# Optimization experiments

Hardware: AMD Instinct MI355X
Metric: run time of the kernel (lower is better)

## Reference

```python
import jax, jax.numpy as jnp
import numpy as np

EPS = 1e-5
SLOPE = 0.01  # torch LeakyReLU default negative_slope


def _stage(h, W):
    # h: [B, N, k, Cin]; W: [Cout, Cin] (1x1 conv, no bias)
    h = jnp.einsum('bnkc,oc->bnko', h, W)
    # InstanceNorm2d (affine=False): normalize per (batch, channel) over spatial (N, k)
    mean = jnp.mean(h, axis=(1, 2), keepdims=True)
    var = jnp.var(h, axis=(1, 2), keepdims=True)
    h = (h - mean) * jax.lax.rsqrt(var + EPS)
    return jnp.where(h >= 0, h, SLOPE * h)


def setup_inputs() -> dict:
    key = jax.random.key(0)
    k1, k2, k3, k4, k5 = jax.random.split(key, 5)
    B, N, D, K, C = 8, 4096, 64, 20, 64
    x = jax.random.normal(k1, (B, N, D), dtype=jnp.float32)
    ind = jax.random.randint(k2, (B, N, K), 0, B * N, dtype=jnp.int64)
    W1 = jax.random.normal(k3, (C, 2 * D), dtype=jnp.float32) * 0.05
    W2 = jax.random.normal(k4, (C, C), dtype=jnp.float32) * 0.05
    W3 = jax.random.normal(k5, (C, C), dtype=jnp.float32) * 0.05
    return {"x": x, "ind": ind, "W1": W1, "W2": W2, "W3": W3}


def reference(x, ind, W1, W2, W3):
    B, N, D = x.shape
    k = ind.shape[2]
    # Gather neighbors via global (B*N) indices, as in the torch code
    y = x.reshape(B * N, D)[ind.reshape(B * N, k)].reshape(B, N, k, D)  # [B,N,k,D]
    xe = jnp.broadcast_to(x[:, :, None, :], (B, N, k, D))
    feat = jnp.concatenate([y - xe, xe], axis=3)  # [B,N,k,2D]
    h = _stage(feat, W1)
    h = _stage(h, W2)
    h = _stage(h, W3)
    # max-pool over k neighbors -> [B, N, Cout]
    return jnp.max(h, axis=2)
```

## Files before the change

kernel.cpp:

```cpp
#include <hip/hip_runtime.h>

#define BDIM 8
#define NPTS 4096
#define KNEI 20
#define BN (BDIM*NPTS)
#define NKCNT (NPTS*KNEI)
#define EPSI 1e-5f
#define SLOPE 0.01f

typedef _Float16 half_t;
typedef __attribute__((ext_vector_type(2))) _Float16 h2v;
typedef __attribute__((ext_vector_type(4))) _Float16 h4v;
typedef __attribute__((ext_vector_type(8))) _Float16 h8v;
typedef __attribute__((ext_vector_type(4))) float f32x4;
typedef __attribute__((ext_vector_type(2))) float f32x2;

__device__ __forceinline__ h2v cvt2(float a, float b) {
    return __builtin_bit_cast(h2v, __builtin_amdgcn_cvt_pkrtz(a, b));
}
__device__ __forceinline__ unsigned long long pack4_f16(const f32x4& a) {
    unsigned p0 = __builtin_bit_cast(unsigned, cvt2(a[0], a[1]));
    unsigned p1 = __builtin_bit_cast(unsigned, cvt2(a[2], a[3]));
    return ((unsigned long long)p1 << 32) | p0;
}

__global__ __launch_bounds__(256) void k0_uv(const float* __restrict__ x,
        const float* __restrict__ W1, const float* __restrict__ W2,
        const float* __restrict__ W3, half_t* __restrict__ u,
        half_t* __restrict__ v, half_t* __restrict__ Wh2,
        half_t* __restrict__ Wh3) {
    int tid = threadIdx.x;
    if (blockIdx.x >= BN / 64) {
        const float* src = (blockIdx.x == BN / 64) ? W2 : W3;
        half_t* dst = (blockIdx.x == BN / 64) ? Wh2 : Wh3;
        for (int i = tid; i < 4096; i += 256) dst[i] = (half_t)src[i];
        return;
    }
    int lane = tid & 63, w = tid >> 6;
    int l15 = lane & 15, q = lane >> 4;
    int row = blockIdx.x * 64 + w * 16 + l15;
    h8v bx[2];
#pragma unroll
    for (int kc = 0; kc < 2; ++kc) {
        const float* xp = x + (size_t)row * 64 + kc * 32 + q * 8;
        f32x4 x0 = *(const f32x4*)xp;
        f32x4 x1 = *(const f32x4*)(xp + 4);
        h8v t;
#pragma unroll
        for (int j = 0; j < 4; ++j) { t[j] = (half_t)x0[j]; t[4 + j] = (half_t)x1[j]; }
        bx[kc] = t;
    }
    h8v wa[4][2], wd[4][2];
#pragma unroll
    for (int mt = 0; mt < 4; ++mt)
#pragma unroll
        for (int kc = 0; kc < 2; ++kc) {
            const float* wp = W1 + (mt * 16 + l15) * 128 + kc * 32 + q * 8;
            f32x4 a0 = *(const f32x4*)wp;
            f32x4 a1 = *(const f32x4*)(wp + 4);
            f32x4 b0 = *(const f32x4*)(wp + 64);
            f32x4 b1 = *(const f32x4*)(wp + 68);
            h8v ta, td;
#pragma unroll
            for (int j = 0; j < 4; ++j) {
                ta[j] = (half_t)a0[j]; ta[4 + j] = (half_t)a1[j];
                td[j] = (half_t)(b0[j] - a0[j]); td[4 + j] = (half_t)(b1[j] - a1[j]);
            }
            wa[mt][kc] = ta; wd[mt][kc] = td;
        }
#pragma unroll
    for (int mt = 0; mt < 4; ++mt) {
        f32x4 au = {0.f, 0.f, 0.f, 0.f}, av = {0.f, 0.f, 0.f, 0.f};
        au = __builtin_amdgcn_mfma_f32_16x16x32_f16(wa[mt][0], bx[0], au, 0, 0, 0);
        au = __builtin_amdgcn_mfma_f32_16x16x32_f16(wa[mt][1], bx[1], au, 0, 0, 0);
        av = __builtin_amdgcn_mfma_f32_16x16x32_f16(wd[mt][0], bx[0], av, 0, 0, 0);
        av = __builtin_amdgcn_mfma_f32_16x16x32_f16(wd[mt][1], bx[1], av, 0, 0, 0);
        *(unsigned long long*)(u + (size_t)row * 64 + mt * 16 + q * 4) = pack4_f16(au);
        *(unsigned long long*)(v + (size_t)row * 64 + mt * 16 + q * 4) = pack4_f16(av);
    }
}

__global__ __launch_bounds__(256) void k1_stats1(const half_t* __restrict__ u,
        const half_t* __restrict__ v, const int* __restrict__ ind,
        float* __restrict__ s1) {
    __shared__ float sacc[128];
    int tid = threadIdx.x;
    if (tid < 128) sacc[tid] = 0.f;
    int lane = tid & 63, w = tid >> 6;
    int b = blockIdx.x >> 8;
    int n0 = (blockIdx.x & 255) << 4;
    int p = b * NPTS + n0 + w * 4 + (lane >> 4);
    int rh = (lane >> 3) & 1, c8 = lane & 7;
    const int* ip = ind + (size_t)p * 20;
    int idx[10];
#pragma unroll
    for (int r = 0; r < 10; ++r) idx[r] = ip[r * 2 + rh];
    h8v vv = *(const h8v*)(v + (size_t)p * 64 + c8 * 8);
    h8v g[10];
#pragma unroll
    for (int r = 0; r < 10; ++r)
        g[r] = *(const h8v*)(u + (size_t)idx[r] * 64 + c8 * 8);
    float s[8] = {}, qa[8] = {};
#pragma unroll
    for (int r = 0; r < 10; ++r) {
        h8v h = g[r] + vv;
#pragma unroll
        for (int j = 0; j < 8; ++j) {
            float f = (float)h[j];
            s[j] += f; qa[j] = fmaf(f, f, qa[j]);
        }
    }
#pragma unroll
    for (int m = 8; m <= 32; m <<= 1)
#pragma unroll
        for (int j = 0; j < 8; ++j) {
            s[j] += __shfl_xor(s[j], m, 64);
            qa[j] += __shfl_xor(qa[j], m, 64);
        }
    __syncthreads();
    if ((lane & 56) == 0) {
#pragma unroll
        for (int j = 0; j < 8; ++j) {
            atomicAdd(&sacc[c8 * 8 + j], s[j]);
            atomicAdd(&sacc[64 + c8 * 8 + j], qa[j]);
        }
    }
    __syncthreads();
    if (tid < 128)
        atomicAdd(&s1[(tid >> 6) * 512 + b * 64 + (tid & 63)], sacc[tid]);
}

__global__ __launch_bounds__(256, 3) void k2_stats2(const half_t* __restrict__ u,
        const half_t* __restrict__ v, const int* __restrict__ ind,
        const half_t* __restrict__ Wh2, const float* __restrict__ s1,
        float* __restrict__ s2) {
    __shared__ float sacc[128];
    int tid = threadIdx.x;
    if (tid < 128) sacc[tid] = 0.f;
    int lane = tid & 63, w = tid >> 6;
    int l15 = lane & 15, q = lane >> 4;
    int b = blockIdx.x >> 8;
    int n0 = (blockIdx.x & 255) << 4;
    int base = b * NPTS + n0;
    int base20 = base * 20;
    int idxs[5];
#pragma unroll
    for (int nt = 0; nt < 5; ++nt)
        idxs[nt] = ind[base20 + w * 80 + l15 * 5 + nt];
    const half_t* up0 = u + (size_t)idxs[0] * 64 + q * 8;
    h8v cu0 = *(const h8v*)up0;
    h8v cu1 = *(const h8v*)(up0 + 32);
    int gp = base + w * 4 + (l15 >> 2);
    h8v vfr[2];
#pragma unroll
    for (int kc = 0; kc < 2; ++kc)
        vfr[kc] = *(const h8v*)(v + (size_t)gp * 64 + kc * 32 + q * 8);
    h8v aw[4][2];
#pragma unroll
    for (int mt = 0; mt < 4; ++mt)
#pragma unroll
        for (int kc = 0; kc < 2; ++kc)
            aw[mt][kc] = *(const h8v*)(Wh2 + (mt * 16 + l15) * 64 + kc * 32 + q * 8);
    const float inv = 1.0f / (float)NKCNT;
    h8v r1v[2], vn[2];
#pragma unroll
    for (int kc = 0; kc < 2; ++kc)
#pragma unroll
        for (int j = 0; j < 8; ++j) {
            int c = kc * 32 + q * 8 + j;
            float mm = s1[b * 64 + c] * inv;
            float va = s1[512 + b * 64 + c] * inv - mm * mm;
            float rs = rsqrtf(va + EPSI);
            r1v[kc][j] = (half_t)rs;
            vn[kc][j] = (half_t)(((float)vfr[kc][j] - mm) * rs);
        }
    float ss[4][4] = {}, sq[4][4] = {};
#pragma unroll
    for (int nt = 0; nt < 5; ++nt) {
        h8v nx0, nx1;
        if (nt < 4) {
            const half_t* upn = u + (size_t)idxs[nt + 1] * 64 + q * 8;
            nx0 = *(const h8v*)upn;
            nx1 = *(const h8v*)(upn + 32);
        }
        h8v t0 = cu0 * r1v[0] + vn[0];
        h8v t1 = cu1 * r1v[1] + vn[1];
        h8v b0 = __builtin_elementwise_max(t0, t0 * (half_t)SLOPE);
        h8v b1 = __builtin_elementwise_max(t1, t1 * (half_t)SLOPE);
#pragma unroll
        for (int mt = 0; mt < 4; ++mt) {
            f32x4 a = {0.f, 0.f, 0.f, 0.f};
            a = __builtin_amdgcn_mfma_f32_16x16x32_f16(aw[mt][0], b0, a, 0, 0, 0);
            a = __builtin_amdgcn_mfma_f32_16x16x32_f16(aw[mt][1], b1, a, 0, 0, 0);
#pragma unroll
            for (int j = 0; j < 4; ++j) {
                ss[mt][j] += a[j];
                sq[mt][j] = fmaf(a[j], a[j], sq[mt][j]);
            }
        }
        if (nt < 4) { cu0 = nx0; cu1 = nx1; }
    }
#pragma unroll
    for (int m = 1; m < 16; m <<= 1)
#pragma unroll
        for (int mt = 0; mt < 4; ++mt)
#pragma unroll
            for (int j = 0; j < 4; ++j) {
                ss[mt][j] += __shfl_xor(ss[mt][j], m, 64);
                sq[mt][j] += __shfl_xor(sq[mt][j], m, 64);
            }
    __syncthreads();
    if (l15 == 0) {
#pragma unroll
        for (int mt = 0; mt < 4; ++mt)
#pragma unroll
            for (int j = 0; j < 4; ++j) {
                atomicAdd(&sacc[mt * 16 + q * 4 + j], ss[mt][j]);
                atomicAdd(&sacc[64 + mt * 16 + q * 4 + j], sq[mt][j]);
            }
    }
    __syncthreads();
    if (tid < 128)
        atomicAdd(&s2[(tid >> 6) * 512 + b * 64 + (tid & 63)], sacc[tid]);
}

__global__ __launch_bounds__(256, 3) void k3_fused(const half_t* __restrict__ u,
        const half_t* __restrict__ v, const int* __restrict__ ind,
        const half_t* __restrict__ Wh2, const half_t* __restrict__ Wh3,
        const float* __restrict__ s1, const float* __restrict__ s2,
        float* __restrict__ s3, float* __restrict__ out) {
    __shared__ __align__(16) unsigned char wlds[16384];
    __shared__ __align__(16) unsigned char scr[16384];
    __shared__ float sacc[128];
    int tid = threadIdx.x;
    if (tid < 128) sacc[tid] = 0.f;
    int lane = tid & 63, w = tid >> 6;
    int l15 = lane & 15, q = lane >> 4;
    int rw7 = l15 & 7;
    int b = blockIdx.x >> 8;
    int n0 = (blockIdx.x & 255) << 4;
    int base = b * NPTS + n0;
    int base20 = base * 20;
    for (int i = tid; i < 512; i += 256) {
        int rw = i >> 3, ch = i & 7;
        *(h8v*)(wlds + rw * 128 + ((ch ^ (rw & 7)) << 4)) =
            *(const h8v*)(Wh2 + rw * 64 + ch * 8);
        *(h8v*)(wlds + 8192 + rw * 128 + ((ch ^ (rw & 7)) << 4)) =
            *(const h8v*)(Wh3 + rw * 64 + ch * 8);
    }
    int idxs[5];
#pragma unroll
    for (int nt = 0; nt < 5; ++nt)
        idxs[nt] = ind[base20 + w * 80 + l15 * 5 + nt];
    const half_t* up0 = u + (size_t)idxs[0] * 64 + q * 8;
    h8v cu0 = *(const h8v*)up0;
    h8v cu1 = *(const h8v*)(up0 + 32);
    int gp = base + w * 4 + (l15 >> 2);
    h8v vfr[2];
#pragma unroll
    for (int kc = 0; kc < 2; ++kc)
        vfr[kc] = *(const h8v*)(v + (size_t)gp * 64 + kc * 32 + q * 8);
    const float inv = 1.0f / (float)NKCNT;
    h8v r1v[2], vn[2], r2v[2], m2v[2];
#pragma unroll
    for (int kc = 0; kc < 2; ++kc)
#pragma unroll
        for (int j = 0; j < 8; ++j) {
            int c = kc * 32 + q * 8 + j;
            float mm = s1[b * 64 + c] * inv;
            float va = s1[512 + b * 64 + c] * inv - mm * mm;
            float rs = rsqrtf(va + EPSI);
            r1v[kc][j] = (half_t)rs;
            vn[kc][j] = (half_t)(((float)vfr[kc][j] - mm) * rs);
            float mm2 = s2[b * 64 + c] * inv;
            float va2 = s2[512 + b * 64 + c] * inv - mm2 * mm2;
            float rs2 = rsqrtf(va2 + EPSI);
            r2v[kc][j] = (half_t)rs2;
            m2v[kc][j] = (half_t)(-mm2 * rs2);
        }
    unsigned char* scrw0 = scr + w * 4096;
    __syncthreads();
    float ss[4][4] = {}, sq[4][4] = {};
    h2v pm[4][2];
#pragma unroll
    for (int mt = 0; mt < 4; ++mt)
#pragma unroll
        for (int r = 0; r < 2; ++r)
            pm[mt][r] = (h2v){(half_t)-65504.f, (half_t)-65504.f};
#pragma unroll
    for (int nt = 0; nt < 6; ++nt) {
        if (nt < 5) {
            h8v nx0, nx1;
            if (nt < 4) {
                const half_t* upn = u + (size_t)idxs[nt + 1] * 64 + q * 8;
                nx0 = *(const h8v*)upn;
                nx1 = *(const h8v*)(upn + 32);
            }
            unsigned char* scrw = scrw0 + (nt & 1) * 2048;
            h8v t0 = cu0 * r1v[0] + vn[0];
            h8v t1 = cu1 * r1v[1] + vn[1];
            h8v b0 = __builtin_elementwise_max(t0, t0 * (half_t)SLOPE);
            h8v b1 = __builtin_elementwise_max(t1, t1 * (half_t)SLOPE);
#pragma unroll
            for (int mt = 0; mt < 4; ++mt) {
                h8v w0 = *(const h8v*)(wlds + (mt * 16 + l15) * 128 + ((q ^ rw7) << 4));
                h8v w1 = *(const h8v*)(wlds + (mt * 16 + l15) * 128 + (((4 + q) ^ rw7) << 4));
                f32x4 a = {0.f, 0.f, 0.f, 0.f};
                a = __builtin_amdgcn_mfma_f32_16x16x32_f16(w0, b0, a, 0, 0, 0);
                a = __builtin_amdgcn_mfma_f32_16x16x32_f16(w1, b1, a, 0, 0, 0);
                *(unsigned long long*)(scrw + l15 * 128 +
                    (((mt * 2 + (q >> 1)) ^ rw7) << 4) + (q & 1) * 8) = pack4_f16(a);
            }
            if (nt < 4) { cu0 = nx0; cu1 = nx1; }
        }
        if (nt > 0) {
            int m = nt - 1;
            unsigned char* scrr = scrw0 + (m & 1) * 2048;
            h8v hr0 = *(const h8v*)(scrr + l15 * 128 + ((q ^ rw7) << 4));
            h8v hr1 = *(const h8v*)(scrr + l15 * 128 + (((4 + q) ^ rw7) << 4));
            h8v t0 = hr0 * r2v[0] + m2v[0];
            h8v t1 = hr1 * r2v[1] + m2v[1];
            h8v b0 = __builtin_elementwise_max(t0, t0 * (half_t)SLOPE);
            h8v b1 = __builtin_elementwise_max(t1, t1 * (half_t)SLOPE);
#pragma unroll
            for (int mt = 0; mt < 4; ++mt) {
                h8v w0 = *(const h8v*)(wlds + 8192 + (mt * 16 + l15) * 128 + ((q ^ rw7) << 4));
                h8v w1 = *(const h8v*)(wlds + 8192 + (mt * 16 + l15) * 128 + (((4 + q) ^ rw7) << 4));
                f32x4 a = {0.f, 0.f, 0.f, 0.f};
                a = __builtin_amdgcn_mfma_f32_16x16x32_f16(w0, b0, a, 0, 0, 0);
                a = __builtin_amdgcn_mfma_f32_16x16x32_f16(w1, b1, a, 0, 0, 0);
#pragma unroll
                for (int j = 0; j < 4; ++j) {
                    ss[mt][j] += a[j];
                    sq[mt][j] = fmaf(a[j], a[j], sq[mt][j]);
                }
                h2v p0 = cvt2(a[0], a[1]);
                h2v p1 = cvt2(a[2], a[3]);
                pm[mt][0] = __builtin_elementwise_max(pm[mt][0], p0);
                pm[mt][1] = __builtin_elementwise_max(pm[mt][1], p1);
            }
        }
    }
#pragma unroll
    for (int m = 1; m <= 2; m <<= 1)
#pragma unroll
        for (int mt = 0; mt < 4; ++mt)
#pragma unroll
            for (int r = 0; r < 2; ++r) {
                int t = __shfl_xor(__builtin_bit_cast(int, pm[mt][r]), m, 64);
                pm[mt][r] = __builtin_elementwise_max(pm[mt][r],
                               __builtin_bit_cast(h2v, t));
            }
    {
        int ms = l15 & 3;
        h2v sa = ms == 0 ? pm[0][0] : ms == 1 ? pm[1][0] : ms == 2 ? pm[2][0] : pm[3][0];
        h2v sb = ms == 0 ? pm[0][1] : ms == 1 ? pm[1][1] : ms == 2 ? pm[2][1] : pm[3][1];
        f32x4 o = {(float)sa[0], (float)sa[1], (float)sb[0], (float)sb[1]};
        *(f32x4*)(out + (size_t)gp * 64 + ms * 16 + q * 4) = o;
    }
#pragma unroll
    for (int m = 1; m < 16; m <<= 1)
#pragma unroll
        for (int mt = 0; mt < 4; ++mt)
#pragma unroll
            for (int j = 0; j < 4; ++j) {
                ss[mt][j] += __shfl_xor(ss[mt][j], m, 64);
                sq[mt][j] += __shfl_xor(sq[mt][j], m, 64);
            }
    if (l15 == 0) {
#pragma unroll
        for (int mt = 0; mt < 4; ++mt)
#pragma unroll
            for (int j = 0; j < 4; ++j) {
                atomicAdd(&sacc[mt * 16 + q * 4 + j], ss[mt][j]);
                atomicAdd(&sacc[64 + mt * 16 + q * 4 + j], sq[mt][j]);
            }
    }
    __syncthreads();
    if (tid < 128)
        atomicAdd(&s3[(tid >> 6) * 512 + b * 64 + (tid & 63)], sacc[tid]);
}

__global__ __launch_bounds__(256) void k4_final(float* __restrict__ out,
        const float* __restrict__ s3) {
    int idx = blockIdx.x * 256 + threadIdx.x;
    int c = idx & 63;
    int b = idx >> 18;
    const float inv = 1.0f / (float)NKCNT;
    float mm = s3[b * 64 + c] * inv;
    float vv = s3[512 + b * 64 + c] * inv - mm * mm;
    float r = rsqrtf(vv + EPSI);
    float val = (out[idx] - mm) * r;
    out[idx] = val >= 0.f ? val : SLOPE * val;
}

extern "C" void kernel_launch(void* const* d_in, const int* in_sizes, int n_in,
                              void* d_out, int out_size, void* d_ws, size_t ws_size,
                              hipStream_t stream) {
    const float* x   = (const float*)d_in[0];
    const int*   ind = (const int*)d_in[1];
    const float* W1  = (const float*)d_in[2];
    const float* W2  = (const float*)d_in[3];
    const float* W3  = (const float*)d_in[4];
    float* out = (float*)d_out;

    half_t* u   = (half_t*)d_ws;
    half_t* v   = u + (size_t)BN * 64;
    half_t* Wh2 = v + (size_t)BN * 64;
    half_t* Wh3 = Wh2 + 4096;
    float* stats = (float*)(Wh3 + 4096);
    float* s1 = stats;
    float* s2 = stats + 1024;
    float* s3 = stats + 2048;

    (void)hipMemsetAsync(stats, 0, 3 * 1024 * sizeof(float), stream);
    k0_uv<<<dim3(BN / 64 + 2), dim3(256), 0, stream>>>(x, W1, W2, W3, u, v, Wh2, Wh3);
    k1_stats1<<<dim3(BN / 16), dim3(256), 0, stream>>>(u, v, ind, s1);
    k2_stats2<<<dim3(BN / 16), dim3(256), 0, stream>>>(u, v, ind, Wh2, s1, s2);
    k3_fused<<<dim3(BN / 16), dim3(256), 0, stream>>>(u, v, ind, Wh2, Wh3, s1, s2, s3, out);
    k4_final<<<dim3(BN * 64 / 256), dim3(256), 0, stream>>>(out, s3);
}
```

Measured before the change: 180.0 us.

## Process two point groups per block with cross-group prefetch in gather kernels

Each block of the three gather kernels now handles two consecutive 16-point groups, so half as many blocks are launched. This amortises the weight loads, the LDS weight staging and the per-block stat atomics. The next group's indices, v rows and first u rows are prefetched during the current group's loop to hide gather latency. The cost is more live registers, which may lower occupancy, and fewer blocks to fill the GPU.

```diff
diff --git a/kernel.cpp b/kernel.cpp
--- a/kernel.cpp
+++ b/kernel.cpp
@@ -87,27 +87,41 @@
     int tid = threadIdx.x;
     if (tid < 128) sacc[tid] = 0.f;
     int lane = tid & 63, w = tid >> 6;
-    int b = blockIdx.x >> 8;
-    int n0 = (blockIdx.x & 255) << 4;
-    int p = b * NPTS + n0 + w * 4 + (lane >> 4);
+    int g0 = blockIdx.x * 2;
+    int b = g0 >> 8;
     int rh = (lane >> 3) & 1, c8 = lane & 7;
-    const int* ip = ind + (size_t)p * 20;
+    int p0 = b * NPTS + ((g0 & 255) << 4) + w * 4 + (lane >> 4);
+    const int* ip = ind + (size_t)p0 * 20;
     int idx[10];
 #pragma unroll
     for (int r = 0; r < 10; ++r) idx[r] = ip[r * 2 + rh];
-    h8v vv = *(const h8v*)(v + (size_t)p * 64 + c8 * 8);
-    h8v g[10];
-#pragma unroll
-    for (int r = 0; r < 10; ++r)
-        g[r] = *(const h8v*)(u + (size_t)idx[r] * 64 + c8 * 8);
     float s[8] = {}, qa[8] = {};
-#pragma unroll
-    for (int r = 0; r < 10; ++r) {
-        h8v h = g[r] + vv;
-#pragma unroll
-        for (int j = 0; j < 8; ++j) {
-            float f = (float)h[j];
-            s[j] += f; qa[j] = fmaf(f, f, qa[j]);
+#pragma unroll 1
+    for (int g = 0; g < 2; ++g) {
+        int p = p0 + g * 16;
+        h8v vv = *(const h8v*)(v + (size_t)p * 64 + c8 * 8);
+        h8v gg[10];
+#pragma unroll
+        for (int r = 0; r < 10; ++r)
+            gg[r] = *(const h8v*)(u + (size_t)idx[r] * 64 + c8 * 8);
+        int idxn[10];
+        if (g == 0) {
+            const int* ipn = ind + (size_t)(p0 + 16) * 20;
+#pragma unroll
+            for (int r = 0; r < 10; ++r) idxn[r] = ipn[r * 2 + rh];
+        }
+#pragma unroll
+        for (int r = 0; r < 10; ++r) {
+            h8v h = gg[r] + vv;
+#pragma unroll
+            for (int j = 0; j < 8; ++j) {
+                float f = (float)h[j];
+                s[j] += f; qa[j] = fmaf(f, f, qa[j]);
+            }
+        }
+        if (g == 0) {
+#pragma unroll
+            for (int r = 0; r < 10; ++r) idx[r] = idxn[r];
         }
     }
 #pragma unroll
@@ -139,22 +153,9 @@
     if (tid < 128) sacc[tid] = 0.f;
     int lane = tid & 63, w = tid >> 6;
     int l15 = lane & 15, q = lane >> 4;
-    int b = blockIdx.x >> 8;
-    int n0 = (blockIdx.x & 255) << 4;
-    int base = b * NPTS + n0;
-    int base20 = base * 20;
-    int idxs[5];
-#pragma unroll
-    for (int nt = 0; nt < 5; ++nt)
-        idxs[nt] = ind[base20 + w * 80 + l15 * 5 + nt];
-    const half_t* up0 = u + (size_t)idxs[0] * 64 + q * 8;
-    h8v cu0 = *(const h8v*)up0;
-    h8v cu1 = *(const h8v*)(up0 + 32);
-    int gp = base + w * 4 + (l15 >> 2);
-    h8v vfr[2];
-#pragma unroll
-    for (int kc = 0; kc < 2; ++kc)
-        vfr[kc] = *(const h8v*)(v + (size_t)gp * 64 + kc * 32 + q * 8);
+    int g0 = blockIdx.x * 2;
+    int b = g0 >> 8;
+    int base0 = b * NPTS + ((g0 & 255) << 4);
     h8v aw[4][2];
 #pragma unroll
     for (int mt = 0; mt < 4; ++mt)
@@ -162,43 +163,77 @@
         for (int kc = 0; kc < 2; ++kc)
             aw[mt][kc] = *(const h8v*)(Wh2 + (mt * 16 + l15) * 64 + kc * 32 + q * 8);
     const float inv = 1.0f / (float)NKCNT;
-    h8v r1v[2], vn[2];
-#pragma unroll
-    for (int kc = 0; kc < 2; ++kc)
-#pragma unroll
-        for (int j = 0; j < 8; ++j) {
-            int c = kc * 32 + q * 8 + j;
-            float mm = s1[b * 64 + c] * inv;
-            float va = s1[512 + b * 64 + c] * inv - mm * mm;
-            float rs = rsqrtf(va + EPSI);
-            r1v[kc][j] = (half_t)rs;
-            vn[kc][j] = (half_t)(((float)vfr[kc][j] - mm) * rs);
-        }
+    int idxs[5];
+#pragma unroll
+    for (int nt = 0; nt < 5; ++nt)
+        idxs[nt] = ind[(size_t)base0 * 20 + w * 80 + l15 * 5 + nt];
+    const half_t* upi = u + (size_t)idxs[0] * 64 + q * 8;
+    h8v cu0 = *(const h8v*)upi;
+    h8v cu1 = *(const h8v*)(upi + 32);
+    int gp0 = base0 + w * 4 + (l15 >> 2);
+    h8v vfr[2];
+    vfr[0] = *(const h8v*)(v + (size_t)gp0 * 64 + q * 8);
+    vfr[1] = *(const h8v*)(v + (size_t)gp0 * 64 + 32 + q * 8);
     float ss[4][4] = {}, sq[4][4] = {};
-#pragma unroll
-    for (int nt = 0; nt < 5; ++nt) {
-        h8v nx0, nx1;
-        if (nt < 4) {
-            const half_t* upn = u + (size_t)idxs[nt + 1] * 64 + q * 8;
-            nx0 = *(const h8v*)upn;
-            nx1 = *(const h8v*)(upn + 32);
-        }
-        h8v t0 = cu0 * r1v[0] + vn[0];
-        h8v t1 = cu1 * r1v[1] + vn[1];
-        h8v b0 = __builtin_elementwise_max(t0, t0 * (half_t)SLOPE);
-        h8v b1 = __builtin_elementwise_max(t1, t1 * (half_t)SLOPE);
-#pragma unroll
-        for (int mt = 0; mt < 4; ++mt) {
-            f32x4 a = {0.f, 0.f, 0.f, 0.f};
-            a = __builtin_amdgcn_mfma_f32_16x16x32_f16(aw[mt][0], b0, a, 0, 0, 0);
-            a = __builtin_amdgcn_mfma_f32_16x16x32_f16(aw[mt][1], b1, a, 0, 0, 0);
-#pragma unroll
-            for (int j = 0; j < 4; ++j) {
-                ss[mt][j] += a[j];
-                sq[mt][j] = fmaf(a[j], a[j], sq[mt][j]);
-            }
-        }
-        if (nt < 4) { cu0 = nx0; cu1 = nx1; }
+#pragma unroll 1
+    for (int g = 0; g < 2; ++g) {
+        h8v r1v[2], vn[2];
+#pragma unroll
+        for (int kc = 0; kc < 2; ++kc)
+#pragma unroll
+            for (int j = 0; j < 8; ++j) {
+                int c = kc * 32 + q * 8 + j;
+                float mm = s1[b * 64 + c] * inv;
+                float va = s1[512 + b * 64 + c] * inv - mm * mm;
+                float rs = rsqrtf(va + EPSI);
+                r1v[kc][j] = (half_t)rs;
+                vn[kc][j] = (half_t)(((float)vfr[kc][j] - mm) * rs);
+            }
+        int idxs_n[5];
+        h8v cun0, cun1, vfn0, vfn1;
+#pragma unroll
+        for (int nt = 0; nt < 5; ++nt) {
+            h8v nx0, nx1;
+            if (nt < 4) {
+                const half_t* upn = u + (size_t)idxs[nt + 1] * 64 + q * 8;
+                nx0 = *(const h8v*)upn;
+                nx1 = *(const h8v*)(upn + 32);
+            }
+            if (nt == 0 && g == 0) {
+#pragma unroll
+                for (int r = 0; r < 5; ++r)
+                    idxs_n[r] = ind[(size_t)(base0 + 16) * 20 + w * 80 + l15 * 5 + r];
+                vfn0 = *(const h8v*)(v + (size_t)(gp0 + 16) * 64 + q * 8);
+                vfn1 = *(const h8v*)(v + (size_t)(gp0 + 16) * 64 + 32 + q * 8);
+            }
+            if (nt == 4 && g == 0) {
+                const half_t* upn = u + (size_t)idxs_n[0] * 64 + q * 8;
+                cun0 = *(const h8v*)upn;
+                cun1 = *(const h8v*)(upn + 32);
+            }
+            h8v t0 = cu0 * r1v[0] + vn[0];
+            h8v t1 = cu1 * r1v[1] + vn[1];
+            h8v b0 = __builtin_elementwise_max(t0, t0 * (half_t)SLOPE);
+            h8v b1 = __builtin_elementwise_max(t1, t1 * (half_t)SLOPE);
+#pragma unroll
+            for (int mt = 0; mt < 4; ++mt) {
+                f32x4 a = {0.f, 0.f, 0.f, 0.f};
+                a = __builtin_amdgcn_mfma_f32_16x16x32_f16(aw[mt][0], b0, a, 0, 0, 0);
+                a = __builtin_amdgcn_mfma_f32_16x16x32_f16(aw[mt][1], b1, a, 0, 0, 0);
+#pragma unroll
+                for (int j = 0; j < 4; ++j) {
+                    ss[mt][j] += a[j];
+                    sq[mt][j] = fmaf(a[j], a[j], sq[mt][j]);
+                }
+            }
+            if (nt < 4) { cu0 = nx0; cu1 = nx1; }
+        }
+        if (g == 0) {
+#pragma unroll
+            for (int r = 0; r < 5; ++r) idxs[r] = idxs_n[r];
+            cu0 = cun0; cu1 = cun1;
+            vfr[0] = vfn0; vfr[1] = vfn1;
+        }
     }
 #pragma unroll
     for (int m = 1; m < 16; m <<= 1)
@@ -237,10 +272,9 @@
     int lane = tid & 63, w = tid >> 6;
     int l15 = lane & 15, q = lane >> 4;
     int rw7 = l15 & 7;
-    int b = blockIdx.x >> 8;
-    int n0 = (blockIdx.x & 255) << 4;
-    int base = b * NPTS + n0;
-    int base20 = base * 20;
+    int g0 = blockIdx.x * 2;
+    int b = g0 >> 8;
+    int base0 = b * NPTS + ((g0 & 255) << 4);
     for (int i = tid; i < 512; i += 256) {
         int rw = i >> 3, ch = i & 7;
         *(h8v*)(wlds + rw * 128 + ((ch ^ (rw & 7)) << 4)) =
@@ -248,115 +282,138 @@
         *(h8v*)(wlds + 8192 + rw * 128 + ((ch ^ (rw & 7)) << 4)) =
             *(const h8v*)(Wh3 + rw * 64 + ch * 8);
     }
+    const float inv = 1.0f / (float)NKCNT;
     int idxs[5];
 #pragma unroll
     for (int nt = 0; nt < 5; ++nt)
-        idxs[nt] = ind[base20 + w * 80 + l15 * 5 + nt];
-    const half_t* up0 = u + (size_t)idxs[0] * 64 + q * 8;
-    h8v cu0 = *(const h8v*)up0;
-    h8v cu1 = *(const h8v*)(up0 + 32);
-    int gp = base + w * 4 + (l15 >> 2);
+        idxs[nt] = ind[(size_t)base0 * 20 + w * 80 + l15 * 5 + nt];
+    const half_t* upi = u + (size_t)idxs[0] * 64 + q * 8;
+    h8v cu0 = *(const h8v*)upi;
+    h8v cu1 = *(const h8v*)(upi + 32);
+    int gp0 = base0 + w * 4 + (l15 >> 2);
     h8v vfr[2];
-#pragma unroll
-    for (int kc = 0; kc < 2; ++kc)
-        vfr[kc] = *(const h8v*)(v + (size_t)gp * 64 + kc * 32 + q * 8);
-    const float inv = 1.0f / (float)NKCNT;
-    h8v r1v[2], vn[2], r2v[2], m2v[2];
-#pragma unroll
-    for (int kc = 0; kc < 2; ++kc)
-#pragma unroll
-        for (int j = 0; j < 8; ++j) {
-            int c = kc * 32 + q * 8 + j;
-            float mm = s1[b * 64 + c] * inv;
-            float va = s1[512 + b * 64 + c] * inv - mm * mm;
-            float rs = rsqrtf(va + EPSI);
-            r1v[kc][j] = (half_t)rs;
-            vn[kc][j] = (half_t)(((float)vfr[kc][j] - mm) * rs);
-            float mm2 = s2[b * 64 + c] * inv;
-            float va2 = s2[512 + b * 64 + c] * inv - mm2 * mm2;
-            float rs2 = rsqrtf(va2 + EPSI);
-            r2v[kc][j] = (half_t)rs2;
-            m2v[kc][j] = (half_t)(-mm2 * rs2);
-        }
+    vfr[0] = *(const h8v*)(v + (size_t)gp0 * 64 + q * 8);
+    vfr[1] = *(const h8v*)(v + (size_t)gp0 * 64 + 32 + q * 8);
     unsigned char* scrw0 = scr + w * 4096;
     __syncthreads();
     float ss[4][4] = {}, sq[4][4] = {};
-    h2v pm[4][2];
-#pragma unroll
-    for (int mt = 0; mt < 4; ++mt)
-#pragma unroll
-        for (int r = 0; r < 2; ++r)
-            pm[mt][r] = (h2v){(half_t)-65504.f, (half_t)-65504.f};
-#pragma unroll
-    for (int nt = 0; nt < 6; ++nt) {
-        if (nt < 5) {
-            h8v nx0, nx1;
-            if (nt < 4) {
-                const half_t* upn = u + (size_t)idxs[nt + 1] * 64 + q * 8;
-                nx0 = *(const h8v*)upn;
-                nx1 = *(const h8v*)(upn + 32);
-            }
-            unsigned char* scrw = scrw0 + (nt & 1) * 2048;
-            h8v t0 = cu0 * r1v[0] + vn[0];
-            h8v t1 = cu1 * r1v[1] + vn[1];
-            h8v b0 = __builtin_elementwise_max(t0, t0 * (half_t)SLOPE);
-            h8v b1 = __builtin_elementwise_max(t1, t1 * (half_t)SLOPE);
-#pragma unroll
-            for (int mt = 0; mt < 4; ++mt) {
-                h8v w0 = *(const h8v*)(wlds + (mt * 16 + l15) * 128 + ((q ^ rw7) << 4));
-                h8v w1 = *(const h8v*)(wlds + (mt * 16 + l15) * 128 + (((4 + q) ^ rw7) << 4));
-                f32x4 a = {0.f, 0.f, 0.f, 0.f};
-                a = __builtin_amdgcn_mfma_f32_16x16x32_f16(w0, b0, a, 0, 0, 0);
-                a = __builtin_amdgcn_mfma_f32_16x16x32_f16(w1, b1, a, 0, 0, 0);
-                *(unsigned long long*)(scrw + l15 * 128 +
-                    (((mt * 2 + (q >> 1)) ^ rw7) << 4) + (q & 1) * 8) = pack4_f16(a);
-            }
-            if (nt < 4) { cu0 = nx0; cu1 = nx1; }
-        }
-        if (nt > 0) {
-            int m = nt - 1;
-            unsigned char* scrr = scrw0 + (m & 1) * 2048;
-            h8v hr0 = *(const h8v*)(scrr + l15 * 128 + ((q ^ rw7) << 4));
-            h8v hr1 = *(const h8v*)(scrr + l15 * 128 + (((4 + q) ^ rw7) << 4));
-            h8v t0 = hr0 * r2v[0] + m2v[0];
-            h8v t1 = hr1 * r2v[1] + m2v[1];
-            h8v b0 = __builtin_elementwise_max(t0, t0 * (half_t)SLOPE);
-            h8v b1 = __builtin_elementwise_max(t1, t1 * (half_t)SLOPE);
-#pragma unroll
-            for (int mt = 0; mt < 4; ++mt) {
-                h8v w0 = *(const h8v*)(wlds + 8192 + (mt * 16 + l15) * 128 + ((q ^ rw7) << 4));
-                h8v w1 = *(const h8v*)(wlds + 8192 + (mt * 16 + l15) * 128 + (((4 + q) ^ rw7) << 4));
-                f32x4 a = {0.f, 0.f, 0.f, 0.f};
-                a = __builtin_amdgcn_mfma_f32_16x16x32_f16(w0, b0, a, 0, 0, 0);
-                a = __builtin_amdgcn_mfma_f32_16x16x32_f16(w1, b1, a, 0, 0, 0);
-#pragma unroll
-                for (int j = 0; j < 4; ++j) {
-                    ss[mt][j] += a[j];
-                    sq[mt][j] = fmaf(a[j], a[j], sq[mt][j]);
-                }
-                h2v p0 = cvt2(a[0], a[1]);
-                h2v p1 = cvt2(a[2], a[3]);
-                pm[mt][0] = __builtin_elementwise_max(pm[mt][0], p0);
-                pm[mt][1] = __builtin_elementwise_max(pm[mt][1], p1);
-            }
-        }
-    }
-#pragma unroll
-    for (int m = 1; m <= 2; m <<= 1)
+#pragma unroll 1
+    for (int g = 0; g < 2; ++g) {
+        int gp = gp0 + g * 16;
+        h8v r1v[2], vn[2], r2v[2], m2v[2];
+#pragma unroll
+        for (int kc = 0; kc < 2; ++kc)
+#pragma unroll
+            for (int j = 0; j < 8; ++j) {
+                int c = kc * 32 + q * 8 + j;
+                float mm = s1[b * 64 + c] * inv;
+                float va = s1[512 + b * 64 + c] * inv - mm * mm;
+                float rs = rsqrtf(va + EPSI);
+                r1v[kc][j] = (half_t)rs;
+                vn[kc][j] = (half_t)(((float)vfr[kc][j] - mm) * rs);
+                float mm2 = s2[b * 64 + c] * inv;
+                float va2 = s2[512 + b * 64 + c] * inv - mm2 * mm2;
+                float rs2 = rsqrtf(va2 + EPSI);
+                r2v[kc][j] = (half_t)rs2;
+                m2v[kc][j] = (half_t)(-mm2 * rs2);
+            }
+        h2v pm[4][2];
 #pragma unroll
         for (int mt = 0; mt < 4; ++mt)
 #pragma unroll
-            for (int r = 0; r < 2; ++r) {
-                int t = __shfl_xor(__builtin_bit_cast(int, pm[mt][r]), m, 64);
-                pm[mt][r] = __builtin_elementwise_max(pm[mt][r],
-                               __builtin_bit_cast(h2v, t));
-            }
-    {
-        int ms = l15 & 3;
-        h2v sa = ms == 0 ? pm[0][0] : ms == 1 ? pm[1][0] : ms == 2 ? pm[2][0] : pm[3][0];
-        h2v sb = ms == 0 ? pm[0][1] : ms == 1 ? pm[1][1] : ms == 2 ? pm[2][1] : pm[3][1];
-        f32x4 o = {(float)sa[0], (float)sa[1], (float)sb[0], (float)sb[1]};
-        *(f32x4*)(out + (size_t)gp * 64 + ms * 16 + q * 4) = o;
+            for (int r = 0; r < 2; ++r)
+                pm[mt][r] = (h2v){(half_t)-65504.f, (half_t)-65504.f};
+        int idxs_n[5];
+        h8v cun0, cun1, vfn0, vfn1;
+#pragma unroll
+        for (int nt = 0; nt < 6; ++nt) {
+            if (nt < 5) {
+                h8v nx0, nx1;
+                if (nt < 4) {
+                    const half_t* upn = u + (size_t)idxs[nt + 1] * 64 + q * 8;
+                    nx0 = *(const h8v*)upn;
+                    nx1 = *(const h8v*)(upn + 32);
+                }
+                if (nt == 0 && g == 0) {
+#pragma unroll
+                    for (int r = 0; r < 5; ++r)
+                        idxs_n[r] = ind[(size_t)(base0 + 16) * 20 + w * 80 + l15 * 5 + r];
+                    vfn0 = *(const h8v*)(v + (size_t)(gp0 + 16) * 64 + q * 8);
+                    vfn1 = *(const h8v*)(v + (size_t)(gp0 + 16) * 64 + 32 + q * 8);
+                }
+                if (nt == 4 && g == 0) {
+                    const half_t* upn = u + (size_t)idxs_n[0] * 64 + q * 8;
+                    cun0 = *(const h8v*)upn;
+                    cun1 = *(const h8v*)(upn + 32);
+                }
+                unsigned char* scrw = scrw0 + (nt & 1) * 2048;
+                h8v t0 = cu0 * r1v[0] + vn[0];
+                h8v t1 = cu1 * r1v[1] + vn[1];
+                h8v b0 = __builtin_elementwise_max(t0, t0 * (half_t)SLOPE);
+                h8v b1 = __builtin_elementwise_max(t1, t1 * (half_t)SLOPE);
+#pragma unroll
+                for (int mt = 0; mt < 4; ++mt) {
+                    h8v w0 = *(const h8v*)(wlds + (mt * 16 + l15) * 128 + ((q ^ rw7) << 4));
+                    h8v w1 = *(const h8v*)(wlds + (mt * 16 + l15) * 128 + (((4 + q) ^ rw7) << 4));
+                    f32x4 a = {0.f, 0.f, 0.f, 0.f};
+                    a = __builtin_amdgcn_mfma_f32_16x16x32_f16(w0, b0, a, 0, 0, 0);
+                    a = __builtin_amdgcn_mfma_f32_16x16x32_f16(w1, b1, a, 0, 0, 0);
+                    *(unsigned long long*)(scrw + l15 * 128 +
+                        (((mt * 2 + (q >> 1)) ^ rw7) << 4) + (q & 1) * 8) = pack4_f16(a);
+                }
+                if (nt < 4) { cu0 = nx0; cu1 = nx1; }
+            }
+            if (nt > 0) {
+                int m = nt - 1;
+                unsigned char* scrr = scrw0 + (m & 1) * 2048;
+                h8v hr0 = *(const h8v*)(scrr + l15 * 128 + ((q ^ rw7) << 4));
+                h8v hr1 = *(const h8v*)(scrr + l15 * 128 + (((4 + q) ^ rw7) << 4));
+                h8v t0 = hr0 * r2v[0] + m2v[0];
+                h8v t1 = hr1 * r2v[1] + m2v[1];
+                h8v b0 = __builtin_elementwise_max(t0, t0 * (half_t)SLOPE);
+                h8v b1 = __builtin_elementwise_max(t1, t1 * (half_t)SLOPE);
+#pragma unroll
+                for (int mt = 0; mt < 4; ++mt) {
+                    h8v w0 = *(const h8v*)(wlds + 8192 + (mt * 16 + l15) * 128 + ((q ^ rw7) << 4));
+                    h8v w1 = *(const h8v*)(wlds + 8192 + (mt * 16 + l15) * 128 + (((4 + q) ^ rw7) << 4));
+                    f32x4 a = {0.f, 0.f, 0.f, 0.f};
+                    a = __builtin_amdgcn_mfma_f32_16x16x32_f16(w0, b0, a, 0, 0, 0);
+                    a = __builtin_amdgcn_mfma_f32_16x16x32_f16(w1, b1, a, 0, 0, 0);
+#pragma unroll
+                    for (int j = 0; j < 4; ++j) {
+                        ss[mt][j] += a[j];
+                        sq[mt][j] = fmaf(a[j], a[j], sq[mt][j]);
+                    }
+                    h2v p0 = cvt2(a[0], a[1]);
+                    h2v p1 = cvt2(a[2], a[3]);
+                    pm[mt][0] = __builtin_elementwise_max(pm[mt][0], p0);
+                    pm[mt][1] = __builtin_elementwise_max(pm[mt][1], p1);
+                }
+            }
+        }
+#pragma unroll
+        for (int m = 1; m <= 2; m <<= 1)
+#pragma unroll
+            for (int mt = 0; mt < 4; ++mt)
+#pragma unroll
+                for (int r = 0; r < 2; ++r) {
+                    int t = __shfl_xor(__builtin_bit_cast(int, pm[mt][r]), m, 64);
+                    pm[mt][r] = __builtin_elementwise_max(pm[mt][r],
+                                   __builtin_bit_cast(h2v, t));
+                }
+        {
+            int ms = l15 & 3;
+            h2v sa = ms == 0 ? pm[0][0] : ms == 1 ? pm[1][0] : ms == 2 ? pm[2][0] : pm[3][0];
+            h2v sb = ms == 0 ? pm[0][1] : ms == 1 ? pm[1][1] : ms == 2 ? pm[2][1] : pm[3][1];
+            f32x4 o = {(float)sa[0], (float)sa[1], (float)sb[0], (float)sb[1]};
+            *(f32x4*)(out + (size_t)gp * 64 + ms * 16 + q * 4) = o;
+        }
+        if (g == 0) {
+#pragma unroll
+            for (int r = 0; r < 5; ++r) idxs[r] = idxs_n[r];
+            cu0 = cun0; cu1 = cun1;
+            vfr[0] = vfn0; vfr[1] = vfn1;
+        }
     }
 #pragma unroll
     for (int m = 1; m < 16; m <<= 1)
@@ -415,8 +472,8 @@
 
     (void)hipMemsetAsync(stats, 0, 3 * 1024 * sizeof(float), stream);
     k0_uv<<<dim3(BN / 64 + 2), dim3(256), 0, stream>>>(x, W1, W2, W3, u, v, Wh2, Wh3);
-    k1_stats1<<<dim3(BN / 16), dim3(256), 0, stream>>>(u, v, ind, s1);
-    k2_stats2<<<dim3(BN / 16), dim3(256), 0, stream>>>(u, v, ind, Wh2, s1, s2);
-    k3_fused<<<dim3(BN / 16), dim3(256), 0, stream>>>(u, v, ind, Wh2, Wh3, s1, s2, s3, out);
+    k1_stats1<<<dim3(BN / 32), dim3(256), 0, stream>>>(u, v, ind, s1);
+    k2_stats2<<<dim3(BN / 32), dim3(256), 0, stream>>>(u, v, ind, Wh2, s1, s2);
+    k3_fused<<<dim3(BN / 32), dim3(256), 0, stream>>>(u, v, ind, Wh2, Wh3, s1, s2, s3, out);
     k4_final<<<dim3(BN * 64 / 256), dim3(256), 0, stream>>>(out, s3);
 }
```

Result: slower. 488.2 us (+171.2%).
